# Performance work log

Hardware: AMD Instinct MI355X
Metric: run time of the kernel (lower is better)

Reference implementation:

```python
import jax, jax.numpy as jnp
import numpy as np

R_MAX = 6.0
P = 3.0


def _envelope(distance, r_max=R_MAX, p=P):
    d = distance / r_max
    env = (1.0
           - (p + 1.0) * (p + 2.0) / 2.0 * d ** p
           + p * (p + 2.0) * d ** (p + 1.0)
           - p * (p + 1.0) / 2.0 * d ** (p + 2.0))
    return env * (distance < r_max)


def setup_inputs() -> dict:
    key = jax.random.key(0)
    k1, k2, k3, k4, k5 = jax.random.split(key, 5)
    N, K, C, SIZE = 50000, 32, 128, 128
    pair = jax.random.normal(k1, (N, K, C), dtype=jnp.float32)
    pair_update = jax.random.normal(k2, (N, K, SIZE), dtype=jnp.float32)
    neighbours = jax.random.randint(k3, (N, K), 0, N, dtype=jnp.int32)
    pair_mask = jnp.ones((N, K), dtype=bool)
    distance = jax.random.uniform(k4, (N,), dtype=jnp.float32)
    W = jax.random.normal(k5, (C, SIZE), dtype=jnp.float32) / np.sqrt(C)
    return {"pair": pair, "pair_update": pair_update, "neighbours": neighbours,
            "pair_mask": pair_mask, "distance": distance, "W": W}


def reference(pair, pair_update, neighbours, pair_mask, distance, W):
    N, K, _ = pair.shape
    size = W.shape[1]
    # gated message: sigmoid(pair @ W) * pair_update, shape [N, K, size]
    gate = jax.nn.sigmoid(jnp.einsum('nkc,cs->nks', pair, W))
    message = gate * pair_update
    message = jnp.where(pair_mask[..., None], message, 0)
    # polynomial envelope cutoff on per-node distance, broadcast [N,1,1]
    message = message * _envelope(distance)[:, None, None]
    # direction == 'outgoing': scatter-add over neighbour indices
    out = jnp.zeros((N, size), dtype=pair.dtype).at[neighbours].add(message)
    return out
```

## Files before the change

kernel.cpp:

```cpp
#include <hip/hip_runtime.h>
#include <stdint.h>

#define KNBR 32
#define CDIM 128
#define SDIM 128
#define CAP  128

typedef __bf16 bf16x8 __attribute__((ext_vector_type(8)));
typedef unsigned short ushortx8 __attribute__((ext_vector_type(8)));
typedef float f32x4 __attribute__((ext_vector_type(4)));

__device__ __forceinline__ unsigned short f32_bf16(float f) {
    unsigned int u = __builtin_bit_cast(unsigned int, f);
    u += 0x7FFFu + ((u >> 16) & 1u);
    return (unsigned short)(u >> 16);
}

__device__ __forceinline__ float envelope_fac(float dist, int msk) {
    const float d  = dist * (1.0f / 6.0f);
    const float d3 = d * d * d;
    float env = 1.0f - 10.0f * d3 + 15.0f * d3 * d - 6.0f * d3 * d * d;
    env = (dist < 6.0f) ? env : 0.0f;
    return (msk != 0) ? env : 0.0f;
}

__global__ void k_scatter_direct(const int* __restrict__ nbr,
                                 const int* __restrict__ pair_mask,
                                 const float* __restrict__ distance,
                                 int* __restrict__ cnt,
                                 int2* __restrict__ buckets, int np4) {
    const int i = blockIdx.x * blockDim.x + threadIdx.x;
    if (i < np4) {
        const int4 v = ((const int4*)nbr)[i];
        const int4 m = ((const int4*)pair_mask)[i];
        const int e0 = i * 4;
        const int   vv[4] = {v.x, v.y, v.z, v.w};
        const int   mm[4] = {m.x, m.y, m.z, m.w};
#pragma unroll
        for (int j = 0; j < 4; ++j) {
            const float f = envelope_fac(distance[(e0 + j) >> 5], mm[j]);
            const int pos = atomicAdd(&cnt[vv[j]], 1);
            if (pos < CAP)
                buckets[((size_t)vv[j] << 7) + pos] =
                    make_int2(e0 + j, __builtin_bit_cast(int, f));
        }
    }
}

__global__ __launch_bounds__(256, 4)
void k_gather(const float* __restrict__ pair,
              const float* __restrict__ pair_update,
              const float* __restrict__ W,
              const int*   __restrict__ cnt,
              const int2*  __restrict__ elist2,
              float* __restrict__ out,
              int nnodes)
{
    __shared__ uint4 wlds[2048];
    const int tid  = threadIdx.x;
    const int lane = tid & 63;
    const int r16  = lane & 15;
    const int g    = lane >> 4;

    for (int e = tid; e < 2048; e += 256) {
        const int el = e & 63, kk = (e >> 6) & 3, ct = e >> 8;
        const int eg = el >> 4, er = el & 15;
        ushortx8 wb;
#pragma unroll
        for (int j = 0; j < 8; ++j)
            wb[j] = f32_bf16(W[(kk * 32 + eg * 8 + j) * SDIM + ct * 16 + er]);
        wlds[e] = __builtin_bit_cast(uint4, wb);
    }
    __syncthreads();

    const int wave   = (int)((blockIdx.x * blockDim.x + tid) >> 6);
    const int nwaves = (int)((gridDim.x * blockDim.x) >> 6);

    int wbase = 0;

    for (int n0 = wave; n0 < nnodes; n0 += nwaves) {
        const int n    = __builtin_amdgcn_readfirstlane(n0);
        const size_t base = (size_t)n << 7;
        const int dc   = cnt[n];
        const int deg  = (dc < CAP) ? dc : CAP;
        const int ntile = (deg + 15) >> 4;

        float accs[8];
#pragma unroll
        for (int ct = 0; ct < 8; ++ct) accs[ct] = 0.0f;

        int emA = 0; float facA = 0.0f;
        if (ntile > 0) {
            const int2 q = elist2[base + ((r16 < deg) ? r16 : 0)];
            emA  = q.x;
            facA = (r16 < deg) ? __builtin_bit_cast(float, q.y) : 0.0f;
        }

        for (int t = 0; t < ntile; ++t) {
            const int tn = (t + 1 < ntile) ? (t + 1) : t;
            const int slotN = tn * 16 + r16;
            const int2 qN = elist2[base + ((slotN < deg) ? slotN : 0)];
            const int   emN  = qN.x;
            const float facN = (slotN < deg) ? __builtin_bit_cast(float, qN.y) : 0.0f;

            int em_e[4]; float fac_e[4];
#pragma unroll
            for (int reg = 0; reg < 4; ++reg) {
                em_e[reg]  = __shfl(emA,  g * 4 + reg);
                fac_e[reg] = __shfl(facA, g * 4 + reg);
            }

            const float* arow = pair + (size_t)emA * CDIM + g * 8;
            f32x4 av[4][2];
#pragma unroll
            for (int kk = 0; kk < 4; ++kk) {
                av[kk][0] = *(const f32x4*)(arow + kk * 32);
                av[kk][1] = *(const f32x4*)(arow + kk * 32 + 4);
            }

            float puv[4][8];
#pragma unroll
            for (int reg = 0; reg < 4; ++reg) {
                const float* pub = pair_update + (size_t)em_e[reg] * SDIM + r16;
#pragma unroll
                for (int ct = 0; ct < 8; ++ct) puv[reg][ct] = pub[ct * 16];
            }

            bf16x8 afrag[4];
#pragma unroll
            for (int kk = 0; kk < 4; ++kk) {
                ushortx8 ab;
#pragma unroll
                for (int j = 0; j < 4; ++j) ab[j]     = f32_bf16(av[kk][0][j]);
#pragma unroll
                for (int j = 0; j < 4; ++j) ab[4 + j] = f32_bf16(av[kk][1][j]);
                afrag[kk] = __builtin_bit_cast(bf16x8, ab);
            }

            f32x4 acc[8];
#pragma unroll
            for (int ct = 0; ct < 8; ++ct) acc[ct] = (f32x4){0.f, 0.f, 0.f, 0.f};
            asm volatile("" : "+v"(wbase));
#pragma unroll
            for (int kk = 0; kk < 4; ++kk) {
#pragma unroll
                for (int ct = 0; ct < 8; ++ct) {
                    const uint4* wp = (const uint4*)((const char*)wlds + wbase)
                                      + (ct * 4 + kk) * 64 + lane;
                    const bf16x8 b = __builtin_bit_cast(bf16x8, *wp);
                    acc[ct] = __builtin_amdgcn_mfma_f32_16x16x32_bf16(
                        afrag[kk], b, acc[ct], 0, 0, 0);
                }
            }

#pragma unroll
            for (int reg = 0; reg < 4; ++reg) {
#pragma unroll
                for (int ct = 0; ct < 8; ++ct) {
                    const float logit = acc[ct][reg];
                    const float gate  = __builtin_amdgcn_rcpf(1.0f + __expf(-logit));
                    accs[ct] += gate * puv[reg][ct] * fac_e[reg];
                }
            }

            emA = emN; facA = facN;
        }

#pragma unroll
        for (int ct = 0; ct < 8; ++ct) {
            float v = accs[ct];
            v += __shfl_xor(v, 16);
            v += __shfl_xor(v, 32);
            accs[ct] = v;
        }
        float* orow = out + (size_t)n * SDIM;
        orow[lane]      = accs[g];
        orow[lane + 64] = accs[4 + g];
    }
}

__global__ __launch_bounds__(256, 2)
void orb_message_atomic(const float* __restrict__ pair,
                        const float* __restrict__ pair_update,
                        const int*   __restrict__ neighbours,
                        const int*   __restrict__ pair_mask,
                        const float* __restrict__ distance,
                        const float* __restrict__ W,
                        float* __restrict__ out,
                        int ntiles)
{
    const int lane = threadIdx.x & 63;
    const int r16  = lane & 15;
    const int g    = lane >> 4;
    const int wave   = (int)((blockIdx.x * blockDim.x + threadIdx.x) >> 6);
    const int nwaves = (int)((gridDim.x * blockDim.x) >> 6);

    bf16x8 wfrag[8][4];
#pragma unroll
    for (int ct = 0; ct < 8; ++ct)
#pragma unroll
        for (int kk = 0; kk < 4; ++kk) {
            ushortx8 wb;
#pragma unroll
            for (int j = 0; j < 8; ++j)
                wb[j] = f32_bf16(W[(kk * 32 + g * 8 + j) * SDIM + ct * 16 + r16]);
            wfrag[ct][kk] = __builtin_bit_cast(bf16x8, wb);
        }

    for (int t = wave; t < ntiles; t += nwaves) {
        const int p0 = t * 16;
        bf16x8 afrag[4];
        const float* arow = pair + (size_t)(p0 + r16) * CDIM + g * 8;
#pragma unroll
        for (int kk = 0; kk < 4; ++kk) {
            const f32x4 v0 = *(const f32x4*)(arow + kk * 32);
            const f32x4 v1 = *(const f32x4*)(arow + kk * 32 + 4);
            ushortx8 ab;
#pragma unroll
            for (int j = 0; j < 4; ++j) ab[j] = f32_bf16(v0[j]);
#pragma unroll
            for (int j = 0; j < 4; ++j) ab[4 + j] = f32_bf16(v1[j]);
            afrag[kk] = __builtin_bit_cast(bf16x8, ab);
        }
        f32x4 acc[8];
#pragma unroll
        for (int ct = 0; ct < 8; ++ct) acc[ct] = (f32x4){0.f, 0.f, 0.f, 0.f};
#pragma unroll
        for (int kk = 0; kk < 4; ++kk)
#pragma unroll
            for (int ct = 0; ct < 8; ++ct)
                acc[ct] = __builtin_amdgcn_mfma_f32_16x16x32_bf16(
                    afrag[kk], wfrag[ct][kk], acc[ct], 0, 0, 0);
#pragma unroll
        for (int reg = 0; reg < 4; ++reg) {
            const int p   = p0 + g * 4 + reg;
            const int tgt = neighbours[p];
            const float fac = envelope_fac(distance[p >> 5], pair_mask[p]);
            const float* pu = pair_update + (size_t)p * SDIM + r16;
            float* op = out + (size_t)tgt * SDIM + r16;
#pragma unroll
            for (int ct = 0; ct < 8; ++ct) {
                const float logit = acc[ct][reg];
                const float gate  = __builtin_amdgcn_rcpf(1.0f + __expf(-logit));
                unsafeAtomicAdd(op + ct * 16, gate * pu[ct * 16] * fac);
            }
        }
    }
}

extern "C" void kernel_launch(void* const* d_in, const int* in_sizes, int n_in,
                              void* d_out, int out_size, void* d_ws, size_t ws_size,
                              hipStream_t stream) {
    const float* pair        = (const float*)d_in[0];
    const float* pair_update = (const float*)d_in[1];
    const int*   neighbours  = (const int*)d_in[2];
    const int*   pair_mask   = (const int*)d_in[3];
    const float* distance    = (const float*)d_in[4];
    const float* W           = (const float*)d_in[5];
    float* out = (float*)d_out;

    const int N      = in_sizes[4];
    const int npairs = N * KNBR;

    const size_t need = (size_t)N * CAP * sizeof(int2) + (size_t)N * sizeof(int);
    if (ws_size < need || (npairs & 3) != 0) {
        hipMemsetAsync(d_out, 0, (size_t)out_size * sizeof(float), stream);
        orb_message_atomic<<<dim3(512), dim3(256), 0, stream>>>(
            pair, pair_update, neighbours, pair_mask, distance, W, out, npairs / 16);
        return;
    }

    int2* buckets = (int2*)d_ws;
    int*  cnt     = (int*)(buckets + (size_t)N * CAP);

    const int np4 = npairs / 4;

    hipMemsetAsync(cnt, 0, (size_t)N * sizeof(int), stream);
    k_scatter_direct<<<dim3((np4 + 255) / 256), dim3(256), 0, stream>>>(
        neighbours, pair_mask, distance, cnt, buckets, np4);
    k_gather<<<dim3(4096), dim3(256), 0, stream>>>(
        pair, pair_update, W, cnt, buckets, out, N);
}
```

Baseline: 509.1 us.

## Transpose MFMA operands so each lane owns one edge row for vector pair_update loads

Swaps the MFMA A/B operands so the accumulator layout puts one edge per lane column. Each lane can then load pair_update as contiguous float4 vectors from its own edge row, with no shuffles to fetch per-edge indices and factors. The cost is a 4-step cross-lane reduction per accumulator at the end of each node, plus a small LDS staging buffer for the output row. Launch bounds drop to 3 blocks per SM to allow more registers. The LDS handoff within a wave relies on s_waitcnt without an explicit barrier, which assumes lockstep execution within the wave.

```diff
diff --git a/kernel.cpp b/kernel.cpp
--- a/kernel.cpp
+++ b/kernel.cpp
@@ -47,7 +47,7 @@
     }
 }
 
-__global__ __launch_bounds__(256, 4)
+__global__ __launch_bounds__(256, 3)
 void k_gather(const float* __restrict__ pair,
               const float* __restrict__ pair_update,
               const float* __restrict__ W,
@@ -57,10 +57,12 @@
               int nnodes)
 {
     __shared__ uint4 wlds[2048];
+    __shared__ float oshare[4][128];
     const int tid  = threadIdx.x;
     const int lane = tid & 63;
     const int r16  = lane & 15;
     const int g    = lane >> 4;
+    const int wid  = tid >> 6;
 
     for (int e = tid; e < 2048; e += 256) {
         const int el = e & 63, kk = (e >> 6) & 3, ct = e >> 8;
@@ -85,9 +87,9 @@
         const int deg  = (dc < CAP) ? dc : CAP;
         const int ntile = (deg + 15) >> 4;
 
-        float accs[8];
-#pragma unroll
-        for (int ct = 0; ct < 8; ++ct) accs[ct] = 0.0f;
+        f32x4 accs[8];
+#pragma unroll
+        for (int ct = 0; ct < 8; ++ct) accs[ct] = (f32x4){0.f, 0.f, 0.f, 0.f};
 
         int emA = 0; float facA = 0.0f;
         if (ntile > 0) {
@@ -103,37 +105,27 @@
             const int   emN  = qN.x;
             const float facN = (slotN < deg) ? __builtin_bit_cast(float, qN.y) : 0.0f;
 
-            int em_e[4]; float fac_e[4];
-#pragma unroll
-            for (int reg = 0; reg < 4; ++reg) {
-                em_e[reg]  = __shfl(emA,  g * 4 + reg);
-                fac_e[reg] = __shfl(facA, g * 4 + reg);
-            }
-
-            const float* arow = pair + (size_t)emA * CDIM + g * 8;
-            f32x4 av[4][2];
+            const float* arow = pair        + (size_t)emA * CDIM;
+            const float* prow = pair_update + (size_t)emA * SDIM;
+            f32x4 av0[4], av1[4];
 #pragma unroll
             for (int kk = 0; kk < 4; ++kk) {
-                av[kk][0] = *(const f32x4*)(arow + kk * 32);
-                av[kk][1] = *(const f32x4*)(arow + kk * 32 + 4);
-            }
-
-            float puv[4][8];
-#pragma unroll
-            for (int reg = 0; reg < 4; ++reg) {
-                const float* pub = pair_update + (size_t)em_e[reg] * SDIM + r16;
-#pragma unroll
-                for (int ct = 0; ct < 8; ++ct) puv[reg][ct] = pub[ct * 16];
-            }
+                av0[kk] = *(const f32x4*)(arow + kk * 32 + g * 8);
+                av1[kk] = *(const f32x4*)(arow + kk * 32 + g * 8 + 4);
+            }
+            f32x4 puv[8];
+#pragma unroll
+            for (int ct = 0; ct < 8; ++ct)
+                puv[ct] = *(const f32x4*)(prow + ct * 16 + g * 4);
 
             bf16x8 afrag[4];
 #pragma unroll
             for (int kk = 0; kk < 4; ++kk) {
                 ushortx8 ab;
 #pragma unroll
-                for (int j = 0; j < 4; ++j) ab[j]     = f32_bf16(av[kk][0][j]);
-#pragma unroll
-                for (int j = 0; j < 4; ++j) ab[4 + j] = f32_bf16(av[kk][1][j]);
+                for (int j = 0; j < 4; ++j) ab[j]     = f32_bf16(av0[kk][j]);
+#pragma unroll
+                for (int j = 0; j < 4; ++j) ab[4 + j] = f32_bf16(av1[kk][j]);
                 afrag[kk] = __builtin_bit_cast(bf16x8, ab);
             }
 
@@ -147,19 +139,19 @@
                 for (int ct = 0; ct < 8; ++ct) {
                     const uint4* wp = (const uint4*)((const char*)wlds + wbase)
                                       + (ct * 4 + kk) * 64 + lane;
-                    const bf16x8 b = __builtin_bit_cast(bf16x8, *wp);
+                    const bf16x8 wf = __builtin_bit_cast(bf16x8, *wp);
                     acc[ct] = __builtin_amdgcn_mfma_f32_16x16x32_bf16(
-                        afrag[kk], b, acc[ct], 0, 0, 0);
+                        wf, afrag[kk], acc[ct], 0, 0, 0);
                 }
             }
 
 #pragma unroll
-            for (int reg = 0; reg < 4; ++reg) {
-#pragma unroll
-                for (int ct = 0; ct < 8; ++ct) {
+            for (int ct = 0; ct < 8; ++ct) {
+#pragma unroll
+                for (int reg = 0; reg < 4; ++reg) {
                     const float logit = acc[ct][reg];
                     const float gate  = __builtin_amdgcn_rcpf(1.0f + __expf(-logit));
-                    accs[ct] += gate * puv[reg][ct] * fac_e[reg];
+                    accs[ct][reg] += gate * puv[ct][reg] * facA;
                 }
             }
 
@@ -168,14 +160,28 @@
 
 #pragma unroll
         for (int ct = 0; ct < 8; ++ct) {
-            float v = accs[ct];
-            v += __shfl_xor(v, 16);
-            v += __shfl_xor(v, 32);
-            accs[ct] = v;
-        }
+#pragma unroll
+            for (int reg = 0; reg < 4; ++reg) {
+                float v = accs[ct][reg];
+                v += __shfl_xor(v, 1);
+                v += __shfl_xor(v, 2);
+                v += __shfl_xor(v, 4);
+                v += __shfl_xor(v, 8);
+                accs[ct][reg] = v;
+            }
+        }
+
+        if (r16 == 0) {
+#pragma unroll
+            for (int ct = 0; ct < 8; ++ct)
+                *(f32x4*)&oshare[wid][ct * 16 + g * 4] = accs[ct];
+        }
+        __builtin_amdgcn_s_waitcnt(0);
+        const float o0 = oshare[wid][lane];
+        const float o1 = oshare[wid][lane + 64];
         float* orow = out + (size_t)n * SDIM;
-        orow[lane]      = accs[g];
-        orow[lane + 64] = accs[4 + g];
+        orow[lane]      = o0;
+        orow[lane + 64] = o1;
     }
 }
 
```

Result: faster. 483.3 us (-5.1%).
